# Kernel optimization log

Measured on AMD Instinct MI355X. Metric: run time of the kernel, lower is better.

Reference implementation:

```python
import jax, jax.numpy as jnp
import numpy as np
from jax import lax

K = 3          # kernel_size
STRIDE = 1
PAD = 1        # (K-1)//2
C = 64         # channels
GC = 16        # group_channels
G = C // GC    # groups = 4
NS = 1         # new_size = ratio * stride
EPS = 1e-5


def mish(x):
    return x * jnp.tanh(jax.nn.softplus(x))


def setup_inputs() -> dict:
    key = jax.random.key(0)
    ks = jax.random.split(key, 4)
    B, H, W = 2, 256, 256
    c1_in = C * K * 2 + G * K * K      # 420
    c1_out = C * NS * NS // 4          # 16
    return {
        "inputs": jax.random.normal(ks[0], (B, C, H, W), jnp.float32),
        "conv1_w": jax.random.normal(ks[1], (c1_out, c1_in, 1, 1), jnp.float32) * 0.05,
        "conv1_b": jnp.zeros((c1_out,), jnp.float32),
        "conv2_w": jax.random.normal(ks[2], (C // 4, C // 4, 3, 3), jnp.float32) * 0.05,
        "conv2_b": jnp.zeros((C // 4,), jnp.float32),
        "conv3_w": jax.random.normal(ks[3], (G * K * K, C // 4, 1, 1), jnp.float32) * 0.05,
        "conv3_b": jnp.zeros((G * K * K,), jnp.float32),
        "bn_gamma": jnp.ones((c1_out,), jnp.float32),
        "bn_beta": jnp.zeros((c1_out,), jnp.float32),
        "bn_mean": jnp.zeros((c1_out,), jnp.float32),
        "bn_var": jnp.ones((c1_out,), jnp.float32),
    }


def _unfold(x, h, w):
    # torch.nn.Unfold(K, 1, PAD, STRIDE): output channel layout (C, kh, kw)
    xp = jnp.pad(x, ((0, 0), (0, 0), (PAD, PAD), (PAD, PAD)))
    cols = [xp[:, :, ki:ki + (h - 1) * STRIDE + 1:STRIDE,
                     kj:kj + (w - 1) * STRIDE + 1:STRIDE]
            for ki in range(K) for kj in range(K)]
    return jnp.stack(cols, axis=2)  # (b, C, K*K, h, w)


def reference(inputs, conv1_w, conv1_b, conv2_w, conv2_b, conv3_w, conv3_b,
              bn_gamma, bn_beta, bn_mean, bn_var):
    b, _, Wd, Hd = inputs.shape
    h = (Wd + 2 * PAD - K) // STRIDE + 1
    w = (Hd + 2 * PAD - K) // STRIDE + 1
    x = _unfold(inputs, h, w).reshape(b, G, GC, K, K, h, w)
    # multi-axis max pooling over (group_channels, kh, kw)
    m_gc = x.max(axis=2).reshape(b, -1, h, w)  # (b, G*K*K, h, w)
    m_kh = x.max(axis=3).reshape(b, -1, h, w)  # (b, C*K, h, w)
    m_kw = x.max(axis=4).reshape(b, -1, h, w)  # (b, C*K, h, w)
    weight = jnp.concatenate([m_gc, m_kh, m_kw], axis=1)  # (b, 420, h, w)
    # conv1 (1x1) + Mish
    weight = mish(jnp.einsum('bihw,oi->bohw', weight, conv1_w[:, :, 0, 0])
                  + conv1_b[None, :, None, None])                  # (b, 16, h, w)
    c = C // 4
    # rearrange 'b (c n1 n2) h w -> (b h w) c n1 n2'
    wn = weight.reshape(b, c, NS, NS, h, w).transpose(0, 4, 5, 1, 2, 3)
    wn = wn.reshape(b * h * w, c, NS, NS)
    wn = lax.conv_general_dilated(wn, conv2_w, (1, 1), ((1, 1), (1, 1)),
                                  dimension_numbers=('NCHW', 'OIHW', 'NCHW'))
    wn = wn + conv2_b[None, :, None, None]
    # rearrange back '(b h w) c n1 n2 -> b (c n1 n2) h w'
    wn = wn.reshape(b, h, w, c, NS, NS).transpose(0, 3, 4, 5, 1, 2)
    wn = wn.reshape(b, c * NS * NS, h, w)
    # BatchNorm (inference form with running stats)
    scale = bn_gamma / jnp.sqrt(bn_var + EPS)
    wn = wn * scale[None, :, None, None] + (bn_beta - bn_mean * scale)[None, :, None, None]
    weight = weight * mish(wn)
    # conv3 (1x1) -> per-pixel attention logits
    weight = jnp.einsum('bihw,oi->bohw', weight, conv3_w[:, :, 0, 0]) \
             + conv3_b[None, :, None, None]                          # (b, G*K*K, h, w)
    weight = jax.nn.softmax(weight.reshape(b, G, 1, K * K, NS * NS, h, w), axis=3)
    # softmax-weighted patch aggregation
    agg = jnp.sum(x.reshape(b, G, GC, K * K, 1, h, w) * weight, axis=3)  # (b,G,GC,NS^2,h,w)
    # fold with kernel=stride=NS (non-overlapping): pure reshape/transpose
    out = agg.reshape(b, C, NS, NS, h, w).transpose(0, 1, 4, 2, 5, 3)
    return out.reshape(b, C, h * NS, w * NS)
```

## Files before the change

### kernel.cpp

```cpp
#include <hip/hip_runtime.h>
#include <hip/hip_bf16.h>
#include <math.h>

#define Cch 64
#define Hh  256
#define Ww  256
#define HW  (Hh * Ww)

#define WS_WA   0
#define WS_WC2  8192
#define WS_SC   8448
#define WS_OFF  8464

typedef __attribute__((ext_vector_type(8))) short bf16x8;
typedef __attribute__((ext_vector_type(4))) float f32x4;

__device__ __forceinline__ float mishf(float x) {
    float e  = __expf(fminf(x, 15.0f));
    float n  = 1.0f + e;
    float n2 = n * n;
    float t  = __fdividef(n2 - 1.0f, n2 + 1.0f);
    return x > 15.0f ? x : x * t;
}

__device__ __forceinline__ unsigned packbf(float a, float b) {
    unsigned short ua = __builtin_bit_cast(unsigned short, __float2bfloat16(a));
    unsigned short ub = __builtin_bit_cast(unsigned short, __float2bfloat16(b));
    return (unsigned)ua | ((unsigned)ub << 16);
}

__device__ __forceinline__ float conv1_wval(const float* w1, int g, int m, int k) {
    if (k < 96) {
        int cc = k / 6, r = k % 6;
        int col = (r < 3) ? (36 + (g * 16 + cc) * 3 + r)
                          : (228 + (g * 16 + cc) * 3 + (r - 3));
        return w1[m * 420 + col];
    } else if (k < 105) {
        return w1[m * 420 + g * 9 + (k - 96)];
    }
    return 0.0f;
}

__global__ __launch_bounds__(256) void prep_kernel(
    const float* __restrict__ w1, const float* __restrict__ w2,
    const float* __restrict__ b2,
    const float* __restrict__ gamma, const float* __restrict__ beta,
    const float* __restrict__ mean,  const float* __restrict__ var,
    float* __restrict__ ws)
{
    unsigned* wsu = (unsigned*)ws;
    const int tid = threadIdx.x;

    for (int idx = tid; idx < 1024; idx += 256) {
        int lane = idx & 63, s = (idx >> 6) & 3, g = idx >> 8;
        int m = lane & 15, half = lane >> 4;
        unsigned hi[4], lo[4];
        #pragma unroll
        for (int jp = 0; jp < 4; ++jp) {
            float hv[2], lv[2];
            #pragma unroll
            for (int e = 0; e < 2; ++e) {
                int k = 32 * s + half * 8 + jp * 2 + e;
                float v  = conv1_wval(w1, g, m, k);
                float hf = __bfloat162float(__float2bfloat16(v));
                hv[e] = hf;
                lv[e] = v - hf;
            }
            hi[jp] = packbf(hv[0], hv[1]);
            lo[jp] = packbf(lv[0], lv[1]);
        }
        int b0 = WS_WA + idx * 8;
        #pragma unroll
        for (int i = 0; i < 4; ++i) { wsu[b0 + i] = hi[i]; wsu[b0 + 4 + i] = lo[i]; }
    }

    for (int idx = tid; idx < 256; idx += 256) {
        int o = idx / 16, i = idx % 16;
        ws[WS_WC2 + idx] = w2[o * 144 + i * 9 + 4];
    }
    if (tid < 16) {
        float sc = gamma[tid] * rsqrtf(var[tid] + 1e-5f);
        ws[WS_SC + tid]  = sc;
        ws[WS_OFF + tid] = b2[tid] * sc + beta[tid] - mean[tid] * sc;
    }
}

#define LOAD9(dst, cb) do {                              \
    const float* r0_ = (cb) + (size_t)hmc * Ww + w;      \
    const float* r1_ = (cb) + (size_t)h   * Ww + w;      \
    const float* r2_ = (cb) + (size_t)hpc * Ww + w;      \
    dst[0] = r0_[offm]; dst[1] = r0_[0]; dst[2] = r0_[offp]; \
    dst[3] = r1_[offm]; dst[4] = r1_[0]; dst[5] = r1_[offp]; \
    dst[6] = r2_[offm]; dst[7] = r2_[0]; dst[8] = r2_[offp]; \
} while (0)

__global__ __launch_bounds__(256) void revo_kernel(
    const float* __restrict__ in,
    const float* __restrict__ b1,
    const float* __restrict__ w3, const float* __restrict__ b3,
    const float* __restrict__ ws,
    float* __restrict__ out)
{
    const int tid  = threadIdx.x;
    const int g    = __builtin_amdgcn_readfirstlane(tid >> 6);
    const int l    = tid & 63;

    const int bid     = blockIdx.x;
    const int logical = ((bid & 7) << 8) + (bid >> 3);
    const int wseg = logical & 3;
    const int h    = (logical >> 2) & (Hh - 1);
    const int b    = logical >> 10;
    const int w    = wseg * 64 + l;

    __shared__ uint4 feats[4][64][16];
    __shared__ f32x4 lds_y[4][64][4];

    const float* base = in + (size_t)b * Cch * HW;

    const bool okm = (w > 0);
    const bool okp = (w < Ww - 1);
    const int offm = okm ? -1 : 0;
    const int offp = okp ?  1 : 0;

    const int hm = h - 1, hp = h + 1;
    const bool okhm = (hm >= 0), okhp = (hp < Hh);
    const int hmc = okhm ? hm : 0;
    const int hpc = okhp ? hp : Hh - 1;

    float p[9], pn[9], pnn[9];
    float gmax[9];
    unsigned pk[53];

    LOAD9(p,  base + (size_t)(g * 16 + 0) * HW);
    LOAD9(pn, base + (size_t)(g * 16 + 1) * HW);

    #pragma unroll
    for (int cc = 0; cc < 16; ++cc) {
        if (cc < 14) {
            LOAD9(pnn, base + (size_t)(g * 16 + cc + 2) * HW);
        }

        float q[9];
        q[0] = (okhm && okm) ? p[0] : 0.0f;
        q[1] =  okhm         ? p[1] : 0.0f;
        q[2] = (okhm && okp) ? p[2] : 0.0f;
        q[3] =  okm          ? p[3] : 0.0f;
        q[4] =  p[4];
        q[5] =  okp          ? p[5] : 0.0f;
        q[6] = (okhp && okm) ? p[6] : 0.0f;
        q[7] =  okhp         ? p[7] : 0.0f;
        q[8] = (okhp && okp) ? p[8] : 0.0f;

        float mkh0 = fmaxf(fmaxf(q[0], q[3]), q[6]);
        float mkh1 = fmaxf(fmaxf(q[1], q[4]), q[7]);
        float mkh2 = fmaxf(fmaxf(q[2], q[5]), q[8]);
        float mkw0 = fmaxf(fmaxf(q[0], q[1]), q[2]);
        float mkw1 = fmaxf(fmaxf(q[3], q[4]), q[5]);
        float mkw2 = fmaxf(fmaxf(q[6], q[7]), q[8]);

        if (cc == 0) {
            #pragma unroll
            for (int k = 0; k < 9; ++k) gmax[k] = q[k];
        } else {
            #pragma unroll
            for (int k = 0; k < 9; ++k) gmax[k] = fmaxf(gmax[k], q[k]);
        }

        pk[3 * cc + 0] = packbf(mkh0, mkh1);
        pk[3 * cc + 1] = packbf(mkh2, mkw0);
        pk[3 * cc + 2] = packbf(mkw1, mkw2);

        #pragma unroll
        for (int k = 0; k < 9; ++k) { p[k] = pn[k]; pn[k] = pnn[k]; }
    }
    pk[48] = packbf(gmax[0], gmax[1]);
    pk[49] = packbf(gmax[2], gmax[3]);
    pk[50] = packbf(gmax[4], gmax[5]);
    pk[51] = packbf(gmax[6], gmax[7]);
    pk[52] = packbf(gmax[8], 0.0f);

    {
        const int sw = l & 7;
        #pragma unroll
        for (int m = 0; m < 13; ++m) {
            uint4 v; v.x = pk[4*m]; v.y = pk[4*m+1]; v.z = pk[4*m+2]; v.w = pk[4*m+3];
            feats[g][l][m ^ sw] = v;
        }
        uint4 vt; vt.x = pk[52]; vt.y = 0u; vt.z = 0u; vt.w = 0u;
        feats[g][l][13 ^ sw] = vt;
        uint4 vz; vz.x = 0u; vz.y = 0u; vz.z = 0u; vz.w = 0u;
        feats[g][l][14 ^ sw] = vz;
        feats[g][l][15 ^ sw] = vz;
    }

    {
        const uint4* wa = (const uint4*)ws;
        uint4 Ahi[4], Alo[4];
        #pragma unroll
        for (int s = 0; s < 4; ++s) {
            int ix = ((g * 4 + s) * 64 + l) * 2;
            Ahi[s] = wa[ix];
            Alo[s] = wa[ix + 1];
        }

        f32x4 acc[4];
        #pragma unroll
        for (int t = 0; t < 4; ++t) acc[t] = (f32x4){0.f, 0.f, 0.f, 0.f};

        const int ln = l & 15, half = l >> 4, sw = l & 7;
        #pragma unroll
        for (int s = 0; s < 4; ++s) {
            #pragma unroll
            for (int t = 0; t < 4; ++t) {
                uint4 bv = feats[g][16 * t + ln][(4 * s + half) ^ sw];
                acc[t] = __builtin_amdgcn_mfma_f32_16x16x32_bf16(
                    __builtin_bit_cast(bf16x8, Ahi[s]),
                    __builtin_bit_cast(bf16x8, bv), acc[t], 0, 0, 0);
                acc[t] = __builtin_amdgcn_mfma_f32_16x16x32_bf16(
                    __builtin_bit_cast(bf16x8, Alo[s]),
                    __builtin_bit_cast(bf16x8, bv), acc[t], 0, 0, 0);
            }
        }
        #pragma unroll
        for (int t = 0; t < 4; ++t)
            lds_y[g][16 * t + ln][half] = acc[t];
    }
    __syncthreads();

    float feat[16];
    {
        f32x4 rr[4];
        #pragma unroll
        for (int r = 0; r < 4; ++r)
            rr[r] = lds_y[0][l][r] + lds_y[1][l][r] + lds_y[2][l][r] + lds_y[3][l][r];
        #pragma unroll
        for (int o = 0; o < 16; ++o)
            feat[o] = mishf(rr[o >> 2][o & 3] + b1[o]);
    }

    float feat2[16];
    {
        const float* wc2 = ws + WS_WC2;
        const float* sc  = ws + WS_SC;
        const float* off = ws + WS_OFF;
        #pragma unroll
        for (int o = 0; o < 16; ++o) {
            float acc = 0.0f;
            #pragma unroll
            for (int i = 0; i < 16; ++i)
                acc = fmaf(wc2[o * 16 + i], feat[i], acc);
            feat2[o] = feat[o] * mishf(acc * sc[o] + off[o]);
        }
    }

    float att[9];
    {
        float mx = -1e30f;
        #pragma unroll
        for (int k = 0; k < 9; ++k) {
            float acc = b3[g * 9 + k];
            const float* r = w3 + (g * 9 + k) * 16;
            #pragma unroll
            for (int i = 0; i < 16; ++i)
                acc = fmaf(r[i], feat2[i], acc);
            att[k] = acc;
            mx = fmaxf(mx, acc);
        }
        float s = 0.0f;
        #pragma unroll
        for (int k = 0; k < 9; ++k) { att[k] = __expf(att[k] - mx); s += att[k]; }
        float inv = __fdividef(1.0f, s);
        #pragma unroll
        for (int k = 0; k < 9; ++k) att[k] *= inv;
    }

    float* ob = out + (((size_t)b * Cch) * Hh + h) * Ww + w;
    LOAD9(p, base + (size_t)(g * 16) * HW);
    for (int gc = 0; gc < 16; ++gc) {
        if (gc < 15) {
            LOAD9(pn, base + (size_t)(g * 16 + gc + 1) * HW);
        }
        float acc = 0.0f;
        acc = fmaf((okhm && okm) ? p[0] : 0.0f, att[0], acc);
        acc = fmaf( okhm         ? p[1] : 0.0f, att[1], acc);
        acc = fmaf((okhm && okp) ? p[2] : 0.0f, att[2], acc);
        acc = fmaf( okm          ? p[3] : 0.0f, att[3], acc);
        acc = fmaf( p[4],                       att[4], acc);
        acc = fmaf( okp          ? p[5] : 0.0f, att[5], acc);
        acc = fmaf((okhp && okm) ? p[6] : 0.0f, att[6], acc);
        acc = fmaf( okhp         ? p[7] : 0.0f, att[7], acc);
        acc = fmaf((okhp && okp) ? p[8] : 0.0f, att[8], acc);
        ob[(size_t)(g * 16 + gc) * HW] = acc;

        #pragma unroll
        for (int k = 0; k < 9; ++k) p[k] = pn[k];
    }
}

extern "C" void kernel_launch(void* const* d_in, const int* in_sizes, int n_in,
                              void* d_out, int out_size, void* d_ws, size_t ws_size,
                              hipStream_t stream) {
    const float* in    = (const float*)d_in[0];
    const float* w1    = (const float*)d_in[1];
    const float* b1    = (const float*)d_in[2];
    const float* w2    = (const float*)d_in[3];
    const float* b2    = (const float*)d_in[4];
    const float* w3    = (const float*)d_in[5];
    const float* b3    = (const float*)d_in[6];
    const float* gamma = (const float*)d_in[7];
    const float* beta  = (const float*)d_in[8];
    const float* mean  = (const float*)d_in[9];
    const float* var   = (const float*)d_in[10];
    float* out = (float*)d_out;
    float* ws  = (float*)d_ws;

    hipLaunchKernelGGL(prep_kernel, dim3(1), dim3(256), 0, stream,
                       w1, w2, b2, gamma, beta, mean, var, ws);

    hipLaunchKernelGGL(revo_kernel, dim3(2048), dim3(256), 0, stream,
                       in, b1, w3, b3, ws, out);
}
```

Baseline: 96.16 us.

## Shrink LDS and registers: drop group-max from MFMA K, stream feature writes

The 9 group-channel-max terms move out of the padded MFMA K dimension and into a separate scalar FMA path, added into the LDS result with atomics. This cuts K from 128 to 96, which removes a quarter of the MFMAs. Packed bf16 features are now written to LDS in chunks of four channels instead of being held in a 53-register array, and the prefetch depth drops from two channels to one. A single LDS slab per wave is reused for both features and outputs, and launch bounds request 3 blocks per SM. Together these aim at higher occupancy. The costs are LDS atomics, a smaller prefetch distance and an explicit waitcnt barrier.

```diff
diff --git a/kernel.cpp b/kernel.cpp
--- a/kernel.cpp
+++ b/kernel.cpp
@@ -8,9 +8,10 @@
 #define HW  (Hh * Ww)
 
 #define WS_WA   0
-#define WS_WC2  8192
-#define WS_SC   8448
-#define WS_OFF  8464
+#define WS_WGC  6144
+#define WS_WC2  6720
+#define WS_SC   6976
+#define WS_OFF  6992
 
 typedef __attribute__((ext_vector_type(8))) short bf16x8;
 typedef __attribute__((ext_vector_type(4))) float f32x4;
@@ -30,15 +31,10 @@
 }
 
 __device__ __forceinline__ float conv1_wval(const float* w1, int g, int m, int k) {
-    if (k < 96) {
-        int cc = k / 6, r = k % 6;
-        int col = (r < 3) ? (36 + (g * 16 + cc) * 3 + r)
-                          : (228 + (g * 16 + cc) * 3 + (r - 3));
-        return w1[m * 420 + col];
-    } else if (k < 105) {
-        return w1[m * 420 + g * 9 + (k - 96)];
-    }
-    return 0.0f;
+    int cc = k / 6, r = k % 6;
+    int col = (r < 3) ? (36 + (g * 16 + cc) * 3 + r)
+                      : (228 + (g * 16 + cc) * 3 + (r - 3));
+    return w1[m * 420 + col];
 }
 
 __global__ __launch_bounds__(256) void prep_kernel(
@@ -51,8 +47,8 @@
     unsigned* wsu = (unsigned*)ws;
     const int tid = threadIdx.x;
 
-    for (int idx = tid; idx < 1024; idx += 256) {
-        int lane = idx & 63, s = (idx >> 6) & 3, g = idx >> 8;
+    for (int idx = tid; idx < 768; idx += 256) {
+        int g = idx / 192, rem = idx % 192, s = rem / 64, lane = rem % 64;
         int m = lane & 15, half = lane >> 4;
         unsigned hi[4], lo[4];
         #pragma unroll
@@ -74,6 +70,10 @@
         for (int i = 0; i < 4; ++i) { wsu[b0 + i] = hi[i]; wsu[b0 + 4 + i] = lo[i]; }
     }
 
+    for (int idx = tid; idx < 576; idx += 256) {
+        int g = idx / 144, rem = idx % 144, o = rem / 9, k = rem % 9;
+        ws[WS_WGC + idx] = w1[o * 420 + g * 9 + k];
+    }
     for (int idx = tid; idx < 256; idx += 256) {
         int o = idx / 16, i = idx % 16;
         ws[WS_WC2 + idx] = w2[o * 144 + i * 9 + 4];
@@ -94,7 +94,7 @@
     dst[6] = r2_[offm]; dst[7] = r2_[0]; dst[8] = r2_[offp]; \
 } while (0)
 
-__global__ __launch_bounds__(256) void revo_kernel(
+__global__ __launch_bounds__(256, 3) void revo_kernel(
     const float* __restrict__ in,
     const float* __restrict__ b1,
     const float* __restrict__ w3, const float* __restrict__ b3,
@@ -112,8 +112,9 @@
     const int b    = logical >> 10;
     const int w    = wseg * 64 + l;
 
-    __shared__ uint4 feats[4][64][16];
-    __shared__ f32x4 lds_y[4][64][4];
+    __shared__ uint4 lds_raw[3072];
+    uint4* slab  = &lds_raw[g * 768];
+    float* ldsYg = (float*)&lds_raw[g * 768];
 
     const float* base = in + (size_t)b * Cch * HW;
 
@@ -127,17 +128,17 @@
     const int hmc = okhm ? hm : 0;
     const int hpc = okhp ? hp : Hh - 1;
 
-    float p[9], pn[9], pnn[9];
+    float p[9], pn[9];
     float gmax[9];
-    unsigned pk[53];
-
-    LOAD9(p,  base + (size_t)(g * 16 + 0) * HW);
-    LOAD9(pn, base + (size_t)(g * 16 + 1) * HW);
+    unsigned buf[12];
+
+    const float* cb0 = base + (size_t)(g * 16) * HW;
+    LOAD9(p, cb0);
 
     #pragma unroll
     for (int cc = 0; cc < 16; ++cc) {
-        if (cc < 14) {
-            LOAD9(pnn, base + (size_t)(g * 16 + cc + 2) * HW);
+        if (cc < 15) {
+            LOAD9(pn, cb0 + (size_t)(cc + 1) * HW);
         }
 
         float q[9];
@@ -166,39 +167,30 @@
             for (int k = 0; k < 9; ++k) gmax[k] = fmaxf(gmax[k], q[k]);
         }
 
-        pk[3 * cc + 0] = packbf(mkh0, mkh1);
-        pk[3 * cc + 1] = packbf(mkh2, mkw0);
-        pk[3 * cc + 2] = packbf(mkw1, mkw2);
-
-        #pragma unroll
-        for (int k = 0; k < 9; ++k) { p[k] = pn[k]; pn[k] = pnn[k]; }
-    }
-    pk[48] = packbf(gmax[0], gmax[1]);
-    pk[49] = packbf(gmax[2], gmax[3]);
-    pk[50] = packbf(gmax[4], gmax[5]);
-    pk[51] = packbf(gmax[6], gmax[7]);
-    pk[52] = packbf(gmax[8], 0.0f);
-
-    {
-        const int sw = l & 7;
-        #pragma unroll
-        for (int m = 0; m < 13; ++m) {
-            uint4 v; v.x = pk[4*m]; v.y = pk[4*m+1]; v.z = pk[4*m+2]; v.w = pk[4*m+3];
-            feats[g][l][m ^ sw] = v;
-        }
-        uint4 vt; vt.x = pk[52]; vt.y = 0u; vt.z = 0u; vt.w = 0u;
-        feats[g][l][13 ^ sw] = vt;
-        uint4 vz; vz.x = 0u; vz.y = 0u; vz.z = 0u; vz.w = 0u;
-        feats[g][l][14 ^ sw] = vz;
-        feats[g][l][15 ^ sw] = vz;
+        buf[(cc & 3) * 3 + 0] = packbf(mkh0, mkh1);
+        buf[(cc & 3) * 3 + 1] = packbf(mkh2, mkw0);
+        buf[(cc & 3) * 3 + 2] = packbf(mkw1, mkw2);
+
+        if ((cc & 3) == 3) {
+            int j = cc >> 2;
+            uint4 v0; v0.x = buf[0]; v0.y = buf[1];  v0.z = buf[2];  v0.w = buf[3];
+            uint4 v1; v1.x = buf[4]; v1.y = buf[5];  v1.z = buf[6];  v1.w = buf[7];
+            uint4 v2; v2.x = buf[8]; v2.y = buf[9];  v2.z = buf[10]; v2.w = buf[11];
+            slab[l * 12 + ((3 * j + 0) ^ (l & 3))] = v0;
+            slab[l * 12 + ((3 * j + 1) ^ (l & 3))] = v1;
+            slab[l * 12 + ((3 * j + 2) ^ (l & 3))] = v2;
+        }
+
+        #pragma unroll
+        for (int k = 0; k < 9; ++k) p[k] = pn[k];
     }
 
     {
         const uint4* wa = (const uint4*)ws;
-        uint4 Ahi[4], Alo[4];
-        #pragma unroll
-        for (int s = 0; s < 4; ++s) {
-            int ix = ((g * 4 + s) * 64 + l) * 2;
+        uint4 Ahi[3], Alo[3];
+        #pragma unroll
+        for (int s = 0; s < 3; ++s) {
+            int ix = ((g * 3 + s) * 64 + l) * 2;
             Ahi[s] = wa[ix];
             Alo[s] = wa[ix + 1];
         }
@@ -207,12 +199,12 @@
         #pragma unroll
         for (int t = 0; t < 4; ++t) acc[t] = (f32x4){0.f, 0.f, 0.f, 0.f};
 
-        const int ln = l & 15, half = l >> 4, sw = l & 7;
-        #pragma unroll
-        for (int s = 0; s < 4; ++s) {
+        const int ln = l & 15, half = l >> 4;
+        #pragma unroll
+        for (int s = 0; s < 3; ++s) {
             #pragma unroll
             for (int t = 0; t < 4; ++t) {
-                uint4 bv = feats[g][16 * t + ln][(4 * s + half) ^ sw];
+                uint4 bv = slab[(16 * t + ln) * 12 + ((4 * s + half) ^ (ln & 3))];
                 acc[t] = __builtin_amdgcn_mfma_f32_16x16x32_bf16(
                     __builtin_bit_cast(bf16x8, Ahi[s]),
                     __builtin_bit_cast(bf16x8, bv), acc[t], 0, 0, 0);
@@ -221,9 +213,25 @@
                     __builtin_bit_cast(bf16x8, bv), acc[t], 0, 0, 0);
             }
         }
+
+        asm volatile("s_waitcnt lgkmcnt(0)" ::: "memory");
+        __builtin_amdgcn_sched_barrier(0);
+
         #pragma unroll
         for (int t = 0; t < 4; ++t)
-            lds_y[g][16 * t + ln][half] = acc[t];
+            *(f32x4*)&ldsYg[(16 * t + ln) * 20 + half * 4] = acc[t];
+    }
+
+    {
+        const float* wgc = ws + WS_WGC + g * 144;
+        #pragma unroll
+        for (int o = 0; o < 16; ++o) {
+            float term = 0.0f;
+            #pragma unroll
+            for (int k = 0; k < 9; ++k)
+                term = fmaf(wgc[o * 9 + k], gmax[k], term);
+            atomicAdd(&ldsYg[l * 20 + o], term);
+        }
     }
     __syncthreads();
 
@@ -231,8 +239,12 @@
     {
         f32x4 rr[4];
         #pragma unroll
-        for (int r = 0; r < 4; ++r)
-            rr[r] = lds_y[0][l][r] + lds_y[1][l][r] + lds_y[2][l][r] + lds_y[3][l][r];
+        for (int r = 0; r < 4; ++r) {
+            rr[r] = (f32x4){0.f, 0.f, 0.f, 0.f};
+            #pragma unroll
+            for (int gp = 0; gp < 4; ++gp)
+                rr[r] += *(const f32x4*)&((const float*)&lds_raw[gp * 768])[l * 20 + 4 * r];
+        }
         #pragma unroll
         for (int o = 0; o < 16; ++o)
             feat[o] = mishf(rr[o >> 2][o & 3] + b1[o]);
@@ -275,10 +287,10 @@
     }
 
     float* ob = out + (((size_t)b * Cch) * Hh + h) * Ww + w;
-    LOAD9(p, base + (size_t)(g * 16) * HW);
+    LOAD9(p, cb0);
     for (int gc = 0; gc < 16; ++gc) {
         if (gc < 15) {
-            LOAD9(pn, base + (size_t)(g * 16 + gc + 1) * HW);
+            LOAD9(pn, cb0 + (size_t)(gc + 1) * HW);
         }
         float acc = 0.0f;
         acc = fmaf((okhm && okm) ? p[0] : 0.0f, att[0], acc);
```

Result: slower. 129.0 us (+34.1%).

## Stage input rows with halo in LDS and compute features inside the MFMA loop

Applied to the files above, without the earlier changes.

Each block now loads its 16 channels x 3 rows (plus halo columns, zero-padded) into shared memory once. The max-pool features are then computed directly from LDS while building the MFMA B operands, replacing the register-held packed features and the feats LDS array. The final aggregation rereads the staged tile instead of issuing 144 global loads per thread a second time. This cuts redundant global and L2 traffic but increases LDS use and LDS read count, and the group-channel max over 16 channels is recomputed per MFMA tile.

```diff
diff --git a/kernel.cpp b/kernel.cpp
--- a/kernel.cpp
+++ b/kernel.cpp
@@ -7,10 +7,15 @@
 #define Ww  256
 #define HW  (Hh * Ww)
 
-#define WS_WA   0
 #define WS_WC2  8192
 #define WS_SC   8448
 #define WS_OFF  8464
+
+#define SROW 67
+#define SCH  201
+#define SGRP 3216
+#define LDSY 12864
+#define LDS_TOT (12864 + 5120)
 
 typedef __attribute__((ext_vector_type(8))) short bf16x8;
 typedef __attribute__((ext_vector_type(4))) float f32x4;
@@ -29,15 +34,12 @@
     return (unsigned)ua | ((unsigned)ub << 16);
 }
 
-__device__ __forceinline__ float conv1_wval(const float* w1, int g, int m, int k) {
-    if (k < 96) {
-        int cc = k / 6, r = k % 6;
-        int col = (r < 3) ? (36 + (g * 16 + cc) * 3 + r)
-                          : (228 + (g * 16 + cc) * 3 + (r - 3));
-        return w1[m * 420 + col];
-    } else if (k < 105) {
-        return w1[m * 420 + g * 9 + (k - 96)];
-    }
+__device__ __forceinline__ float conv1_wval(const float* w1, int g, int m,
+                                            int cc, int j) {
+    int c = g * 16 + cc;
+    if (j < 3)  return w1[m * 420 + 36 + c * 3 + j];
+    if (j < 6)  return w1[m * 420 + 228 + c * 3 + (j - 3)];
+    if (j == 6) return (cc < 9) ? w1[m * 420 + g * 9 + cc] : 0.0f;
     return 0.0f;
 }
 
@@ -52,16 +54,16 @@
     const int tid = threadIdx.x;
 
     for (int idx = tid; idx < 1024; idx += 256) {
-        int lane = idx & 63, s = (idx >> 6) & 3, g = idx >> 8;
+        int g = idx >> 8, s = (idx >> 6) & 3, lane = idx & 63;
         int m = lane & 15, half = lane >> 4;
+        int cc = 4 * s + half;
         unsigned hi[4], lo[4];
         #pragma unroll
         for (int jp = 0; jp < 4; ++jp) {
             float hv[2], lv[2];
             #pragma unroll
             for (int e = 0; e < 2; ++e) {
-                int k = 32 * s + half * 8 + jp * 2 + e;
-                float v  = conv1_wval(w1, g, m, k);
+                float v  = conv1_wval(w1, g, m, cc, jp * 2 + e);
                 float hf = __bfloat162float(__float2bfloat16(v));
                 hv[e] = hf;
                 lv[e] = v - hf;
@@ -69,7 +71,7 @@
             hi[jp] = packbf(hv[0], hv[1]);
             lo[jp] = packbf(lv[0], lv[1]);
         }
-        int b0 = WS_WA + idx * 8;
+        int b0 = idx * 8;
         #pragma unroll
         for (int i = 0; i < 4; ++i) { wsu[b0 + i] = hi[i]; wsu[b0 + 4 + i] = lo[i]; }
     }
@@ -84,15 +86,6 @@
         ws[WS_OFF + tid] = b2[tid] * sc + beta[tid] - mean[tid] * sc;
     }
 }
-
-#define LOAD9(dst, cb) do {                              \
-    const float* r0_ = (cb) + (size_t)hmc * Ww + w;      \
-    const float* r1_ = (cb) + (size_t)h   * Ww + w;      \
-    const float* r2_ = (cb) + (size_t)hpc * Ww + w;      \
-    dst[0] = r0_[offm]; dst[1] = r0_[0]; dst[2] = r0_[offp]; \
-    dst[3] = r1_[offm]; dst[4] = r1_[0]; dst[5] = r1_[offp]; \
-    dst[6] = r2_[offm]; dst[7] = r2_[0]; dst[8] = r2_[offp]; \
-} while (0)
 
 __global__ __launch_bounds__(256) void revo_kernel(
     const float* __restrict__ in,
@@ -110,88 +103,37 @@
     const int wseg = logical & 3;
     const int h    = (logical >> 2) & (Hh - 1);
     const int b    = logical >> 10;
-    const int w    = wseg * 64 + l;
-
-    __shared__ uint4 feats[4][64][16];
-    __shared__ f32x4 lds_y[4][64][4];
-
-    const float* base = in + (size_t)b * Cch * HW;
-
-    const bool okm = (w > 0);
-    const bool okp = (w < Ww - 1);
-    const int offm = okm ? -1 : 0;
-    const int offp = okp ?  1 : 0;
-
-    const int hm = h - 1, hp = h + 1;
-    const bool okhm = (hm >= 0), okhp = (hp < Hh);
-    const int hmc = okhm ? hm : 0;
-    const int hpc = okhp ? hp : Hh - 1;
-
-    float p[9], pn[9], pnn[9];
-    float gmax[9];
-    unsigned pk[53];
-
-    LOAD9(p,  base + (size_t)(g * 16 + 0) * HW);
-    LOAD9(pn, base + (size_t)(g * 16 + 1) * HW);
-
+    const int wbase = wseg * 64;
+    const int w     = wbase + l;
+
+    __shared__ float lds[LDS_TOT];
+    float* stageg = lds + g * SGRP;
+    float* ldsy   = lds + LDSY;
+
+    const float* base = in + ((size_t)b * Cch + g * 16) * HW;
+
+    {
+        #pragma unroll 6
+        for (int it = 0; it < 48; ++it) {
+            int c = it / 3, r = it % 3;
+            int hr = h + r - 1;
+            float v = 0.0f, vh = 0.0f;
+            if (hr >= 0 && hr < Hh) {
+                const float* rowp = base + (size_t)c * HW + (size_t)hr * Ww;
+                v = rowp[wbase + l];
+                if (l == 0 && wseg > 0)  vh = rowp[wbase - 1];
+                if (l == 63 && wseg < 3) vh = rowp[wbase + 64];
+            }
+            stageg[c * SCH + r * SROW + 1 + l] = v;
+            if (l == 0)  stageg[c * SCH + r * SROW]      = vh;
+            if (l == 63) stageg[c * SCH + r * SROW + 65] = vh;
+        }
+    }
+
+    const int ln = l & 15, half = l >> 4;
+    f32x4 acc[4];
     #pragma unroll
-    for (int cc = 0; cc < 16; ++cc) {
-        if (cc < 14) {
-            LOAD9(pnn, base + (size_t)(g * 16 + cc + 2) * HW);
-        }
-
-        float q[9];
-        q[0] = (okhm && okm) ? p[0] : 0.0f;
-        q[1] =  okhm         ? p[1] : 0.0f;
-        q[2] = (okhm && okp) ? p[2] : 0.0f;
-        q[3] =  okm          ? p[3] : 0.0f;
-        q[4] =  p[4];
-        q[5] =  okp          ? p[5] : 0.0f;
-        q[6] = (okhp && okm) ? p[6] : 0.0f;
-        q[7] =  okhp         ? p[7] : 0.0f;
-        q[8] = (okhp && okp) ? p[8] : 0.0f;
-
-        float mkh0 = fmaxf(fmaxf(q[0], q[3]), q[6]);
-        float mkh1 = fmaxf(fmaxf(q[1], q[4]), q[7]);
-        float mkh2 = fmaxf(fmaxf(q[2], q[5]), q[8]);
-        float mkw0 = fmaxf(fmaxf(q[0], q[1]), q[2]);
-        float mkw1 = fmaxf(fmaxf(q[3], q[4]), q[5]);
-        float mkw2 = fmaxf(fmaxf(q[6], q[7]), q[8]);
-
-        if (cc == 0) {
-            #pragma unroll
-            for (int k = 0; k < 9; ++k) gmax[k] = q[k];
-        } else {
-            #pragma unroll
-            for (int k = 0; k < 9; ++k) gmax[k] = fmaxf(gmax[k], q[k]);
-        }
-
-        pk[3 * cc + 0] = packbf(mkh0, mkh1);
-        pk[3 * cc + 1] = packbf(mkh2, mkw0);
-        pk[3 * cc + 2] = packbf(mkw1, mkw2);
-
-        #pragma unroll
-        for (int k = 0; k < 9; ++k) { p[k] = pn[k]; pn[k] = pnn[k]; }
-    }
-    pk[48] = packbf(gmax[0], gmax[1]);
-    pk[49] = packbf(gmax[2], gmax[3]);
-    pk[50] = packbf(gmax[4], gmax[5]);
-    pk[51] = packbf(gmax[6], gmax[7]);
-    pk[52] = packbf(gmax[8], 0.0f);
-
-    {
-        const int sw = l & 7;
-        #pragma unroll
-        for (int m = 0; m < 13; ++m) {
-            uint4 v; v.x = pk[4*m]; v.y = pk[4*m+1]; v.z = pk[4*m+2]; v.w = pk[4*m+3];
-            feats[g][l][m ^ sw] = v;
-        }
-        uint4 vt; vt.x = pk[52]; vt.y = 0u; vt.z = 0u; vt.w = 0u;
-        feats[g][l][13 ^ sw] = vt;
-        uint4 vz; vz.x = 0u; vz.y = 0u; vz.z = 0u; vz.w = 0u;
-        feats[g][l][14 ^ sw] = vz;
-        feats[g][l][15 ^ sw] = vz;
-    }
+    for (int t = 0; t < 4; ++t) acc[t] = (f32x4){0.f, 0.f, 0.f, 0.f};
 
     {
         const uint4* wa = (const uint4*)ws;
@@ -203,16 +145,42 @@
             Alo[s] = wa[ix + 1];
         }
 
-        f32x4 acc[4];
-        #pragma unroll
-        for (int t = 0; t < 4; ++t) acc[t] = (f32x4){0.f, 0.f, 0.f, 0.f};
-
-        const int ln = l & 15, half = l >> 4, sw = l & 7;
         #pragma unroll
         for (int s = 0; s < 4; ++s) {
+            const int cc = 4 * s + half;
+            const float* chp = stageg + cc * SCH;
+            const bool hasgc = (cc < 9);
+            const int rp = cc / 3, dp = cc % 3;
+
             #pragma unroll
             for (int t = 0; t < 4; ++t) {
-                uint4 bv = feats[g][16 * t + ln][(4 * s + half) ^ sw];
+                const int p = 16 * t + ln;
+                float a0 = chp[p],           a1 = chp[p + 1],       a2 = chp[p + 2];
+                float b0 = chp[SROW + p],    b1v = chp[SROW + p + 1], b2v = chp[SROW + p + 2];
+                float c0 = chp[2*SROW + p],  c1 = chp[2*SROW + p + 1], c2 = chp[2*SROW + p + 2];
+
+                float mkh0 = fmaxf(fmaxf(a0, b0), c0);
+                float mkh1 = fmaxf(fmaxf(a1, b1v), c1);
+                float mkh2 = fmaxf(fmaxf(a2, b2v), c2);
+                float mkw0 = fmaxf(fmaxf(a0, a1), a2);
+                float mkw1 = fmaxf(fmaxf(b0, b1v), b2v);
+                float mkw2 = fmaxf(fmaxf(c0, c1), c2);
+
+                float gv = 0.0f;
+                if (hasgc) {
+                    const float* gp2 = stageg + rp * SROW + dp + p;
+                    gv = gp2[0];
+                    #pragma unroll
+                    for (int c2i = 1; c2i < 16; ++c2i)
+                        gv = fmaxf(gv, gp2[c2i * SCH]);
+                }
+
+                uint4 bv;
+                bv.x = packbf(mkh0, mkh1);
+                bv.y = packbf(mkh2, mkw0);
+                bv.z = packbf(mkw1, mkw2);
+                bv.w = packbf(gv, 0.0f);
+
                 acc[t] = __builtin_amdgcn_mfma_f32_16x16x32_bf16(
                     __builtin_bit_cast(bf16x8, Ahi[s]),
                     __builtin_bit_cast(bf16x8, bv), acc[t], 0, 0, 0);
@@ -221,21 +189,27 @@
                     __builtin_bit_cast(bf16x8, bv), acc[t], 0, 0, 0);
             }
         }
-        #pragma unroll
-        for (int t = 0; t < 4; ++t)
-            lds_y[g][16 * t + ln][half] = acc[t];
-    }
+    }
+
+    #pragma unroll
+    for (int t = 0; t < 4; ++t)
+        *(f32x4*)&ldsy[(g * 64 + 16 * t + ln) * 20 + 4 * half] = acc[t];
     __syncthreads();
 
     float feat[16];
     {
-        f32x4 rr[4];
-        #pragma unroll
-        for (int r = 0; r < 4; ++r)
-            rr[r] = lds_y[0][l][r] + lds_y[1][l][r] + lds_y[2][l][r] + lds_y[3][l][r];
-        #pragma unroll
-        for (int o = 0; o < 16; ++o)
-            feat[o] = mishf(rr[o >> 2][o & 3] + b1[o]);
+        #pragma unroll
+        for (int r4 = 0; r4 < 4; ++r4) {
+            f32x4 rr = (f32x4){0.f, 0.f, 0.f, 0.f};
+            #pragma unroll
+            for (int gp = 0; gp < 4; ++gp)
+                rr += *(const f32x4*)&ldsy[(gp * 64 + l) * 20 + 4 * r4];
+            #pragma unroll
+            for (int j = 0; j < 4; ++j)
+                feat[4 * r4 + j] = rr[j];
+        }
+        #pragma unroll
+        for (int o = 0; o < 16; ++o) feat[o] = mishf(feat[o] + b1[o]);
     }
 
     float feat2[16];
@@ -245,11 +219,11 @@
         const float* off = ws + WS_OFF;
         #pragma unroll
         for (int o = 0; o < 16; ++o) {
-            float acc = 0.0f;
+            float acc2 = 0.0f;
             #pragma unroll
             for (int i = 0; i < 16; ++i)
-                acc = fmaf(wc2[o * 16 + i], feat[i], acc);
-            feat2[o] = feat[o] * mishf(acc * sc[o] + off[o]);
+                acc2 = fmaf(wc2[o * 16 + i], feat[i], acc2);
+            feat2[o] = feat[o] * mishf(acc2 * sc[o] + off[o]);
         }
     }
 
@@ -258,13 +232,13 @@
         float mx = -1e30f;
         #pragma unroll
         for (int k = 0; k < 9; ++k) {
-            float acc = b3[g * 9 + k];
+            float acc2 = b3[g * 9 + k];
             const float* r = w3 + (g * 9 + k) * 16;
             #pragma unroll
             for (int i = 0; i < 16; ++i)
-                acc = fmaf(r[i], feat2[i], acc);
-            att[k] = acc;
-            mx = fmaxf(mx, acc);
+                acc2 = fmaf(r[i], feat2[i], acc2);
+            att[k] = acc2;
+            mx = fmaxf(mx, acc2);
         }
         float s = 0.0f;
         #pragma unroll
@@ -274,26 +248,24 @@
         for (int k = 0; k < 9; ++k) att[k] *= inv;
     }
 
-    float* ob = out + (((size_t)b * Cch) * Hh + h) * Ww + w;
-    LOAD9(p, base + (size_t)(g * 16) * HW);
-    for (int gc = 0; gc < 16; ++gc) {
-        if (gc < 15) {
-            LOAD9(pn, base + (size_t)(g * 16 + gc + 1) * HW);
-        }
-        float acc = 0.0f;
-        acc = fmaf((okhm && okm) ? p[0] : 0.0f, att[0], acc);
-        acc = fmaf( okhm         ? p[1] : 0.0f, att[1], acc);
-        acc = fmaf((okhm && okp) ? p[2] : 0.0f, att[2], acc);
-        acc = fmaf( okm          ? p[3] : 0.0f, att[3], acc);
-        acc = fmaf( p[4],                       att[4], acc);
-        acc = fmaf( okp          ? p[5] : 0.0f, att[5], acc);
-        acc = fmaf((okhp && okm) ? p[6] : 0.0f, att[6], acc);
-        acc = fmaf( okhp         ? p[7] : 0.0f, att[7], acc);
-        acc = fmaf((okhp && okp) ? p[8] : 0.0f, att[8], acc);
-        ob[(size_t)(g * 16 + gc) * HW] = acc;
-
-        #pragma unroll
-        for (int k = 0; k < 9; ++k) p[k] = pn[k];
+    float* ob = out + (((size_t)b * Cch + g * 16) * Hh + h) * Ww + w;
+    #pragma unroll 4
+    for (int c = 0; c < 16; ++c) {
+        const float* chp = stageg + c * SCH;
+        float a0 = chp[l],          a1 = chp[l + 1],          a2 = chp[l + 2];
+        float b0 = chp[SROW + l],   b1v = chp[SROW + l + 1],  b2v = chp[SROW + l + 2];
+        float c0 = chp[2*SROW + l], c1 = chp[2*SROW + l + 1], c2 = chp[2*SROW + l + 2];
+        float acc2 = 0.0f;
+        acc2 = fmaf(a0,  att[0], acc2);
+        acc2 = fmaf(a1,  att[1], acc2);
+        acc2 = fmaf(a2,  att[2], acc2);
+        acc2 = fmaf(b0,  att[3], acc2);
+        acc2 = fmaf(b1v, att[4], acc2);
+        acc2 = fmaf(b2v, att[5], acc2);
+        acc2 = fmaf(c0,  att[6], acc2);
+        acc2 = fmaf(c1,  att[7], acc2);
+        acc2 = fmaf(c2,  att[8], acc2);
+        ob[(size_t)c * HW] = acc2;
     }
 }
 
```

After: 112.6 us. 1.17x slower.
